# Performance work log

Measured on AMD Instinct MI355X. Metric: run time of the kernel, lower is better.

The kernel has to match this reference:

```python
import jax, jax.numpy as jnp
import numpy as np

EPS = 1e-5
K = 9  # 3x3 kernel taps


def _deform_conv_bn_relu(x, w_off, b_off, w, gamma, beta):
    B, C, H, W = x.shape
    dt = x.dtype
    # offset-predicting conv: [B, 2*K, H, W], channel layout (y,x) pairs per tap (mmcv v1)
    offset = jax.lax.conv_general_dilated(
        x, w_off, window_strides=(1, 1), padding=((1, 1), (1, 1)),
        dimension_numbers=('NCHW', 'OIHW', 'NCHW')) + b_off[None, :, None, None]
    off = offset.reshape(B, K, 2, H, W)
    # kernel tap displacements relative to output pixel (padding=1 -> centered 3x3)
    dy = (jnp.arange(K) // 3 - 1).astype(dt)
    dx = (jnp.arange(K) % 3 - 1).astype(dt)
    ii = jnp.arange(H, dtype=dt)[:, None]
    jj = jnp.arange(W, dtype=dt)[None, :]
    py = ii[None, None] + dy[None, :, None, None] + off[:, :, 0]  # [B,K,H,W]
    px = jj[None, None] + dx[None, :, None, None] + off[:, :, 1]
    y0 = jnp.floor(py)
    x0 = jnp.floor(px)
    ly = py - y0
    lx = px - x0

    xf = x.reshape(B, C, H * W)

    def gather(yc, xc, wt):
        # bilinear corner gather with zero padding outside the image
        valid = (yc >= 0) & (yc < H) & (xc >= 0) & (xc < W)
        yi = jnp.clip(yc, 0, H - 1).astype(jnp.int32)
        xi = jnp.clip(xc, 0, W - 1).astype(jnp.int32)
        idx = (yi * W + xi).reshape(B, -1)              # [B, K*H*W]
        g = jax.vmap(lambda xb, ib: xb[:, ib])(xf, idx)  # [B, C, K*H*W]
        wm = (wt * valid.astype(dt)).reshape(B, 1, -1)
        return g * wm

    val = (gather(y0, x0, (1 - ly) * (1 - lx))
           + gather(y0, x0 + 1, (1 - ly) * lx)
           + gather(y0 + 1, x0, ly * (1 - lx))
           + gather(y0 + 1, x0 + 1, ly * lx))
    val = val.reshape(B, C, K, H, W)

    # deformable conv accumulation (no bias in mmcv DeformConv2d v1)
    O = w.shape[0]
    out = jnp.einsum('ock,bckhw->bohw', w.reshape(O, C, K), val)

    # BatchNorm (training-mode batch stats) + ReLU
    mean = out.mean(axis=(0, 2, 3))
    var = out.var(axis=(0, 2, 3))
    out = (out - mean[None, :, None, None]) * jax.lax.rsqrt(var + EPS)[None, :, None, None]
    out = out * gamma[None, :, None, None] + beta[None, :, None, None]
    return jax.nn.relu(out)


def setup_inputs() -> dict:
    key = jax.random.key(0)
    k1, k2, k3 = jax.random.split(key, 3)
    B, C, O, H, W = 2, 256, 256, 128, 128
    x = jax.random.normal(k1, (B, C, H, W), dtype=jnp.float32)
    # offset branch: small init so predicted offsets stay in a realistic range
    w_off = jax.random.normal(k2, (2 * K, C, 3, 3), dtype=jnp.float32) * 0.01
    b_off = jnp.zeros((2 * K,), dtype=jnp.float32)
    w = jax.random.normal(k3, (O, C, 3, 3), dtype=jnp.float32) * 0.05
    gamma = jnp.ones((O,), dtype=jnp.float32)
    beta = jnp.zeros((O,), dtype=jnp.float32)
    return {"x": x, "w_off": w_off, "b_off": b_off, "w": w, "gamma": gamma, "beta": beta}


def reference(x, w_off, b_off, w, gamma, beta):
    return _deform_conv_bn_relu(x, w_off, b_off, w, gamma, beta)
```

## Files before the change

kernel.cpp:

```cpp
#include <hip/hip_runtime.h>
#include <hip/hip_bf16.h>

#define HWs   16384
#define Wimg  128
#define Himg  128
#define PW    130
#define PHW   16900
#define Cin   256
#define Oout  256
#define CKd   2304
#define Bb    2

typedef short   bf16x8 __attribute__((ext_vector_type(8)));
typedef float   f32x4  __attribute__((ext_vector_type(4)));

__device__ __forceinline__ float bf2f(ushort u){
  union { unsigned int i; float f; } v; v.i = ((unsigned int)u) << 16; return v.f;
}
__device__ __forceinline__ ushort f2bf(float f){
  union { float f; unsigned int i; } v; v.f = f;
  return (ushort)((v.i + 0x8000u) >> 16);
}
__device__ __forceinline__ unsigned cvt_pk_bf16(float lo, float hi){
  unsigned r;
  asm("v_cvt_pk_bf16_f32 %0, %1, %2" : "=v"(r) : "v"(lo), "v"(hi));
  return r;
}
__device__ __forceinline__ void gload_lds16(const ushort* g, void* l){
  __builtin_amdgcn_global_load_lds(
      (const __attribute__((address_space(1))) unsigned int*)g,
      (__attribute__((address_space(3))) unsigned int*)l, 16, 0, 0);
}

__global__ __launch_bounds__(256) void k_transpose(const float* __restrict__ x,
                                                   ushort* __restrict__ xtp){
  int bx = blockIdx.x;
  int b  = bx >> 10;
  int r  = bx & 1023;
  int ct = r >> 8;
  int pt = r & 255;
  int c0 = ct * 64, p0 = pt * 64;
  __shared__ float tile[64][65];
  const float* xb = x + (size_t)b * Cin * HWs;
  #pragma unroll
  for (int pass = 0; pass < 16; ++pass){
    int idx = pass * 256 + threadIdx.x;
    int cl = idx >> 6, pl = idx & 63;
    tile[cl][pl] = xb[(size_t)(c0 + cl) * HWs + p0 + pl];
  }
  __syncthreads();
  ushort* xo = xtp + (size_t)b * PHW * Cin;
  #pragma unroll
  for (int pass = 0; pass < 16; ++pass){
    int idx = pass * 256 + threadIdx.x;
    int pl = idx >> 6, cl = idx & 63;
    int hw = p0 + pl; int y = hw >> 7, xc = hw & 127;
    xo[(size_t)((y + 1) * PW + xc + 1) * Cin + c0 + cl] = f2bf(tile[cl][pl]);
  }
}

__global__ __launch_bounds__(64) void k_border(ushort* __restrict__ xtp){
  int e = blockIdx.x;
  int b = e / 516, p = e % 516;
  int y, xc;
  if (p < 130)      { y = 0;       xc = p; }
  else if (p < 260) { y = 129;     xc = p - 130; }
  else if (p < 388) { y = p - 259; xc = 0; }
  else              { y = p - 387; xc = 129; }
  uint2* dst = (uint2*)(xtp + ((size_t)b * PHW + y * PW + xc) * Cin) + threadIdx.x;
  *dst = make_uint2(0u, 0u);
}

__global__ __launch_bounds__(256) void k_wprep(const float* __restrict__ w,
                                               const float* __restrict__ wof,
                                               ushort* __restrict__ w2,
                                               ushort* __restrict__ w2of){
  int idx = blockIdx.x * 256 + threadIdx.x;
  if (idx < Oout * CKd){
    int o = idx / CKd, r = idx % CKd;
    int k = r >> 8, c = r & 255;
    w2[idx] = f2bf(w[(size_t)(o * Cin + c) * 9 + k]);
  } else {
    int j = idx - Oout * CKd;
    int o = j / CKd, r = j % CKd;
    int k = r >> 8, c = r & 255;
    float v = (o < 18) ? wof[(size_t)(o * Cin + c) * 9 + k] : 0.f;
    w2of[j] = f2bf(v);
  }
}

__global__ __launch_bounds__(512, 4) void k_offconv(const ushort* __restrict__ xtp,
                                                    const ushort* __restrict__ w2of,
                                                    const float* __restrict__ b_off,
                                                    int4* __restrict__ pidx,
                                                    float4* __restrict__ pw){
  int bx = blockIdx.x;
  int blkm = ((bx & 7) << 6) | (bx >> 3);
  int b = blkm >> 8, tile = blkm & 255;
  int hw0 = tile * 64;
  int iy = tile >> 1, jx0 = (tile & 1) * 64;
  __shared__ __align__(16) ushort aw[2][2048];
  __shared__ __align__(16) ushort bv_s[2][4096];
  __shared__ float offs_lds[18][64];
  int t = threadIdx.x, lane = t & 63, wid = t >> 6;
  int mi = wid >> 2, ni = wid & 3;
  f32x4 acc = (f32x4){0,0,0,0};
  const ushort* xb = xtp + (size_t)b * PHW * Cin;

#define OSTAGE(S, P) \
  if ((S) < 36){ int kks = (S) * 64, kt = (S) >> 2, c0s = ((S) * 64) & 255; \
    int dy = kt / 3 - 1, dxx = kt % 3 - 1; \
    if (wid < 4){ int L = t * 16; int oo = L >> 7; int inb = (L & 127) ^ ((oo & 7) << 4); \
      gload_lds16(w2of + (size_t)oo * CKd + kks + (inb >> 1), (char*)aw[P] + L); } \
    { int L = t * 16; int hw_l = L >> 7; int inb = (L & 127) ^ ((hw_l & 7) << 4); \
      int row = (iy + dy + 1) * PW + (jx0 + hw_l + dxx + 1); \
      gload_lds16(xb + (size_t)row * Cin + c0s + (inb >> 1), (char*)bv_s[P] + L); } }

  OSTAGE(0, 0);
  __syncthreads();
  #pragma unroll 1
  for (int step = 0; step < 36; ++step){
    int P = step & 1;
    OSTAGE(step + 1, P ^ 1);
    #pragma unroll
    for (int kk2 = 0; kk2 < 2; ++kk2){
      int coff = kk2 * 64 + ((lane >> 4) << 4);
      bf16x8 a0, bb;
      { int r = mi * 16 + (lane & 15); int byte = r * 128 + coff; byte ^= ((r & 7) << 4); a0 = *(const bf16x8*)((char*)aw[P] + byte); }
      { int r = ni * 16 + (lane & 15); int byte = r * 128 + coff; byte ^= ((r & 7) << 4); bb = *(const bf16x8*)((char*)bv_s[P] + byte); }
      acc = __builtin_amdgcn_mfma_f32_16x16x32_bf16(a0, bb, acc, 0, 0, 0);
    }
    __syncthreads();
  }
#undef OSTAGE
  {
    int hw_l = ni * 16 + (lane & 15);
    #pragma unroll
    for (int r = 0; r < 4; ++r){
      int o = mi * 16 + ((lane >> 4) << 2) + r;
      if (o < 18) offs_lds[o][hw_l] = acc[r] + b_off[o];
    }
  }
  __syncthreads();
  for (int idx = t; idx < 9 * 64; idx += 512){
    int k = idx >> 6, jl = idx & 63;
    int hw = hw0 + jl;
    int i = hw >> 7, jcol = hw & 127;
    float offy = offs_lds[2 * k][jl];
    float offx = offs_lds[2 * k + 1][jl];
    float py = (float)i    + (float)(k / 3 - 1) + offy;
    float px = (float)jcol + (float)(k % 3 - 1) + offx;
    float y0f = floorf(py), x0f = floorf(px);
    float ly = py - y0f, lx = px - x0f;
    int y0 = (int)y0f, x0 = (int)x0f;
    int y1 = y0 + 1, x1 = x0 + 1;
    float w00 = (1.f - ly) * (1.f - lx), w01 = (1.f - ly) * lx;
    float w10 = ly * (1.f - lx),         w11 = ly * lx;
    bool vy0 = (y0 >= 0 && y0 < 128), vy1 = (y1 >= 0 && y1 < 128);
    bool vx0 = (x0 >= 0 && x0 < 128), vx1 = (x1 >= 0 && x1 < 128);
    int iy0 = min(max(y0, 0), 127), iy1 = min(max(y1, 0), 127);
    int ix0 = min(max(x0, 0), 127), ix1 = min(max(x1, 0), 127);
    size_t e = ((size_t)b * 9 + k) * HWs + hw;
    pidx[e] = make_int4(((iy0 + 1) * PW + ix0 + 1) * Cin, ((iy0 + 1) * PW + ix1 + 1) * Cin,
                        ((iy1 + 1) * PW + ix0 + 1) * Cin, ((iy1 + 1) * PW + ix1 + 1) * Cin);
    pw[e]   = make_float4(vy0 && vx0 ? w00 : 0.f, vy0 && vx1 ? w01 : 0.f,
                          vy1 && vx0 ? w10 : 0.f, vy1 && vx1 ? w11 : 0.f);
  }
}

__device__ __forceinline__ unsigned combine_pair(unsigned d0, unsigned d1, unsigned d2, unsigned d3,
                                                 float4 wt){
  float e0 = wt.x * __uint_as_float(d0 << 16)
           + wt.y * __uint_as_float(d1 << 16)
           + wt.z * __uint_as_float(d2 << 16)
           + wt.w * __uint_as_float(d3 << 16);
  float e1 = wt.x * __uint_as_float(d0 & 0xFFFF0000u)
           + wt.y * __uint_as_float(d1 & 0xFFFF0000u)
           + wt.z * __uint_as_float(d2 & 0xFFFF0000u)
           + wt.w * __uint_as_float(d3 & 0xFFFF0000u);
  return cvt_pk_bf16(e0, e1);
}

__global__ __launch_bounds__(512, 2) void k_main(const ushort* __restrict__ xtp,
                                                 const ushort* __restrict__ w2,
                                                 const int4* __restrict__ pidx,
                                                 const float4* __restrict__ pw,
                                                 float* __restrict__ out,
                                                 float* __restrict__ partials){
  int bx = blockIdx.x;
  int blkm = ((bx & 7) << 5) | (bx >> 3);
  int b = blkm >> 7, tile = blkm & 127;
  int hw0 = tile * 128;
  __shared__ __align__(16) ushort smem[49152];
  ushort* Ab0 = smem;
  ushort* Ab1 = smem + 16384;
  ushort* Bb0 = smem + 32768;
  ushort* Bb1 = smem + 40960;
  int t = threadIdx.x, lane = t & 63, wid = t >> 6;
  int wm = wid >> 1, wn = wid & 1;
  int cg = t & 7, hl = t >> 3;
  f32x4 acc[4][4];
  #pragma unroll
  for (int mi = 0; mi < 4; ++mi)
    #pragma unroll
    for (int ni = 0; ni < 4; ++ni) acc[mi][ni] = (f32x4){0,0,0,0};
  const ushort* xb  = xtp  + (size_t)b * PHW * Cin;
  const int4*   pib = pidx + (size_t)b * 9 * HWs + hw0;
  const float4* pwb = pw   + (size_t)b * 9 * HWs + hw0;

  int4   ids[2][2];
  float4 wts[2][2];
  uint4  g[2][2][4];

#define IDSLOAD(P, S) \
  if ((S) < 36){ int kq = (S) >> 2; \
    ids[P][0] = pib[(size_t)kq * HWs + hl]; \
    ids[P][1] = pib[(size_t)kq * HWs + hl + 64]; }

#define CORNERS(P, S) \
  if ((S) < 36){ int cb = (((S) * 64) & 255) + cg * 8; int kq = (S) >> 2; \
    wts[P][0] = pwb[(size_t)kq * HWs + hl]; \
    wts[P][1] = pwb[(size_t)kq * HWs + hl + 64]; \
    _Pragma("unroll") for (int hh = 0; hh < 2; ++hh){ \
      g[P][hh][0] = *(const uint4*)(xb + ids[P][hh].x + cb); \
      g[P][hh][1] = *(const uint4*)(xb + ids[P][hh].y + cb); \
      g[P][hh][2] = *(const uint4*)(xb + ids[P][hh].z + cb); \
      g[P][hh][3] = *(const uint4*)(xb + ids[P][hh].w + cb); } }

#define STAGEA(S, ABP) \
  if ((S) < 36){ int kks = (S) * 64; \
    _Pragma("unroll") for (int h2 = 0; h2 < 4; ++h2){ \
      int L = (wid * 4 + h2) * 1024 + lane * 16; \
      int oo = L >> 7; int inb = (L & 127) ^ ((oo & 7) << 4); \
      gload_lds16(w2 + (size_t)oo * CKd + kks + (inb >> 1), (char*)(ABP) + L); } }

#define COMBINE(P, S, BBP) \
  if ((S) < 36){ \
    _Pragma("unroll") for (int hh = 0; hh < 2; ++hh){ \
      int hw_l = hl + hh * 64; \
      float4 wtv = wts[P][hh]; \
      uint4 ov; \
      ov.x = combine_pair(g[P][hh][0].x, g[P][hh][1].x, g[P][hh][2].x, g[P][hh][3].x, wtv); \
      ov.y = combine_pair(g[P][hh][0].y, g[P][hh][1].y, g[P][hh][2].y, g[P][hh][3].y, wtv); \
      ov.z = combine_pair(g[P][hh][0].z, g[P][hh][1].z, g[P][hh][2].z, g[P][hh][3].z, wtv); \
      ov.w = combine_pair(g[P][hh][0].w, g[P][hh][1].w, g[P][hh][2].w, g[P][hh][3].w, wtv); \
      int byte = hw_l * 128 + cg * 16; byte ^= ((hw_l & 7) << 4); \
      *(uint4*)((char*)(BBP) + byte) = ov; } }

#define MFMA_PHASE(ABP, BBP) \
  { __builtin_amdgcn_s_setprio(1); \
    _Pragma("unroll") for (int kk2 = 0; kk2 < 2; ++kk2){ \
      int coff = kk2 * 64 + ((lane >> 4) << 4); \
      bf16x8 a[4], bv[4]; \
      _Pragma("unroll") for (int mi = 0; mi < 4; ++mi){ \
        int r = wm * 64 + mi * 16 + (lane & 15); \
        int byte = r * 128 + coff; byte ^= ((r & 7) << 4); \
        a[mi] = *(const bf16x8*)((const char*)(ABP) + byte); } \
      _Pragma("unroll") for (int ni = 0; ni < 4; ++ni){ \
        int r = wn * 64 + ni * 16 + (lane & 15); \
        int byte = r * 128 + coff; byte ^= ((r & 7) << 4); \
        bv[ni] = *(const bf16x8*)((const char*)(BBP) + byte); } \
      _Pragma("unroll") for (int mi = 0; mi < 4; ++mi) \
        _Pragma("unroll") for (int ni = 0; ni < 4; ++ni) \
          acc[mi][ni] = __builtin_amdgcn_mfma_f32_16x16x32_bf16(a[mi], bv[ni], acc[mi][ni], 0, 0, 0); } \
    __builtin_amdgcn_s_setprio(0); }

  IDSLOAD(0, 0);
  IDSLOAD(1, 1);
  CORNERS(0, 0);
  IDSLOAD(0, 2);
  CORNERS(1, 1);
  IDSLOAD(1, 3);
  STAGEA(0, Ab0);
  COMBINE(0, 0, Bb0);
  __syncthreads();

  #pragma unroll 1
  for (int tt = 0; tt < 36; tt += 2){
    CORNERS(0, tt + 2);
    STAGEA(tt + 1, Ab1);
    IDSLOAD(0, tt + 4);
    MFMA_PHASE(Ab0, Bb0);
    COMBINE(1, tt + 1, Bb1);
    __syncthreads();
    CORNERS(1, tt + 3);
    STAGEA(tt + 2, Ab0);
    IDSLOAD(1, tt + 5);
    MFMA_PHASE(Ab1, Bb1);
    COMBINE(0, tt + 2, Bb0);
    __syncthreads();
  }
#undef IDSLOAD
#undef CORNERS
#undef STAGEA
#undef COMBINE
#undef MFMA_PHASE

  #pragma unroll
  for (int mi = 0; mi < 4; ++mi){
    int obase = wm * 64 + mi * 16 + ((lane >> 4) << 2);
    #pragma unroll
    for (int ni = 0; ni < 4; ++ni){
      int hw = hw0 + wn * 64 + ni * 16 + (lane & 15);
      float* op = out + ((size_t)b * Oout + obase) * HWs + hw;
      #pragma unroll
      for (int r = 0; r < 4; ++r) op[(size_t)r * HWs] = acc[mi][ni][r];
    }
  }
  #pragma unroll
  for (int mi = 0; mi < 4; ++mi){
    #pragma unroll
    for (int r = 0; r < 4; ++r){
      float s = 0.f, s2 = 0.f;
      #pragma unroll
      for (int ni = 0; ni < 4; ++ni){ float v = acc[mi][ni][r]; s += v; s2 += v * v; }
      #pragma unroll
      for (int off2 = 1; off2 < 16; off2 <<= 1){
        s  += __shfl_xor(s, off2);
        s2 += __shfl_xor(s2, off2);
      }
      if ((lane & 15) == 0){
        int o = wm * 64 + mi * 16 + ((lane >> 4) << 2) + r;
        int row = blkm * 2 + wn;
        partials[(size_t)row * 256 + o] = s;
        partials[(size_t)512 * 256 + (size_t)row * 256 + o] = s2;
      }
    }
  }
}

__global__ __launch_bounds__(256) void k_bnstats(const float* __restrict__ partials,
                                                 float* __restrict__ stats){
  int o = blockIdx.x, t = threadIdx.x;
  float s = 0.f, s2 = 0.f;
  for (int i = t; i < 512; i += 256){
    s  += partials[(size_t)i * 256 + o];
    s2 += partials[(size_t)512 * 256 + (size_t)i * 256 + o];
  }
  #pragma unroll
  for (int off = 32; off > 0; off >>= 1){
    s  += __shfl_down(s, off);
    s2 += __shfl_down(s2, off);
  }
  __shared__ float rs[4], rs2[4];
  int lane = t & 63, w = t >> 6;
  if (lane == 0){ rs[w] = s; rs2[w] = s2; }
  __syncthreads();
  if (t == 0){
    float S = 0.f, S2 = 0.f;
    for (int i = 0; i < 4; ++i){ S += rs[i]; S2 += rs2[i]; }
    float mean = S / 32768.f;
    float var  = S2 / 32768.f - mean * mean;
    stats[o] = mean;
    stats[256 + o] = rsqrtf(var + 1e-5f);
  }
}

__global__ __launch_bounds__(256) void k_bnapply(float* __restrict__ out,
                                                 const float* __restrict__ stats,
                                                 const float* __restrict__ gamma,
                                                 const float* __restrict__ beta){
  size_t e = ((size_t)blockIdx.x * 256 + threadIdx.x) * 4;
  int o = (int)((e >> 14) & 255);
  float mean = stats[o], rstd = stats[256 + o];
  float sc = rstd * gamma[o];
  float sh = beta[o] - mean * sc;
  float4 v = *(float4*)(out + e);
  v.x = fmaxf(v.x * sc + sh, 0.f);
  v.y = fmaxf(v.y * sc + sh, 0.f);
  v.z = fmaxf(v.z * sc + sh, 0.f);
  v.w = fmaxf(v.w * sc + sh, 0.f);
  *(float4*)(out + e) = v;
}

extern "C" void kernel_launch(void* const* d_in, const int* in_sizes, int n_in,
                              void* d_out, int out_size, void* d_ws, size_t ws_size,
                              hipStream_t stream){
  const float* x     = (const float*)d_in[0];
  const float* w_off = (const float*)d_in[1];
  const float* b_off = (const float*)d_in[2];
  const float* w     = (const float*)d_in[3];
  const float* gamma = (const float*)d_in[4];
  const float* beta  = (const float*)d_in[5];
  float* out = (float*)d_out;

  char* p = (char*)d_ws;
  ushort* xtp  = (ushort*)p; p += (size_t)Bb * PHW * Cin * 2;
  ushort* w2   = (ushort*)p; p += (size_t)Oout * CKd * 2;
  ushort* w2of = (ushort*)p; p += (size_t)32 * CKd * 2;
  int4*   pidx = (int4*)p;   p += (size_t)Bb * 9 * HWs * 16;
  float4* pwt  = (float4*)p; p += (size_t)Bb * 9 * HWs * 16;
  float*  parts= (float*)p;  p += (size_t)2 * 512 * 256 * 4;
  float*  stats= (float*)p;

  k_transpose<<<dim3(2048), dim3(256), 0, stream>>>(x, xtp);
  k_border   <<<dim3(1032), dim3(64),  0, stream>>>(xtp);
  k_wprep    <<<dim3(2592), dim3(256), 0, stream>>>(w, w_off, w2, w2of);
  k_offconv  <<<dim3(512),  dim3(512), 0, stream>>>(xtp, w2of, b_off, pidx, pwt);
  k_main     <<<dim3(256),  dim3(512), 0, stream>>>(xtp, w2, pidx, pwt, out, parts);
  k_bnstats  <<<dim3(256),  dim3(256), 0, stream>>>(parts, stats);
  k_bnapply  <<<dim3(8192), dim3(256), 0, stream>>>(out, stats, gamma, beta);
}
```

Before: 126.0 us.

## Double k_main block to 1024 threads, halving per-thread gather and MFMA work

The main deformable-conv GEMM kernel now launches 1024 threads (16 waves in a 4x4 wave grid) instead of 512. Each thread gathers one pixel instead of two and holds a 4x2 accumulator tile instead of 4x4. The BN partials buffer and the stats reduction grow to 1024 rows to match. The aim is more waves in flight to hide gather latency and lower register pressure, at the cost of less B-fragment reuse per wave and more LDS reads per MFMA.

```diff
diff --git a/kernel.cpp b/kernel.cpp
--- a/kernel.cpp
+++ b/kernel.cpp
@@ -181,12 +181,12 @@
   return cvt_pk_bf16(e0, e1);
 }
 
-__global__ __launch_bounds__(512, 2) void k_main(const ushort* __restrict__ xtp,
-                                                 const ushort* __restrict__ w2,
-                                                 const int4* __restrict__ pidx,
-                                                 const float4* __restrict__ pw,
-                                                 float* __restrict__ out,
-                                                 float* __restrict__ partials){
+__global__ __launch_bounds__(1024, 4) void k_main(const ushort* __restrict__ xtp,
+                                                  const ushort* __restrict__ w2,
+                                                  const int4* __restrict__ pidx,
+                                                  const float4* __restrict__ pw,
+                                                  float* __restrict__ out,
+                                                  float* __restrict__ partials){
   int bx = blockIdx.x;
   int blkm = ((bx & 7) << 5) | (bx >> 3);
   int b = blkm >> 7, tile = blkm & 127;
@@ -197,71 +197,66 @@
   ushort* Bb0 = smem + 32768;
   ushort* Bb1 = smem + 40960;
   int t = threadIdx.x, lane = t & 63, wid = t >> 6;
-  int wm = wid >> 1, wn = wid & 1;
+  int wm = wid >> 2, wn = wid & 3;
   int cg = t & 7, hl = t >> 3;
-  f32x4 acc[4][4];
+  f32x4 acc[4][2];
   #pragma unroll
   for (int mi = 0; mi < 4; ++mi)
     #pragma unroll
-    for (int ni = 0; ni < 4; ++ni) acc[mi][ni] = (f32x4){0,0,0,0};
+    for (int ni = 0; ni < 2; ++ni) acc[mi][ni] = (f32x4){0,0,0,0};
   const ushort* xb  = xtp  + (size_t)b * PHW * Cin;
   const int4*   pib = pidx + (size_t)b * 9 * HWs + hw0;
   const float4* pwb = pw   + (size_t)b * 9 * HWs + hw0;
 
-  int4   ids[2][2];
-  float4 wts[2][2];
-  uint4  g[2][2][4];
+  int4   ids[2];
+  float4 wts[2];
+  uint4  g[2][4];
 
 #define IDSLOAD(P, S) \
   if ((S) < 36){ int kq = (S) >> 2; \
-    ids[P][0] = pib[(size_t)kq * HWs + hl]; \
-    ids[P][1] = pib[(size_t)kq * HWs + hl + 64]; }
+    ids[P] = pib[(size_t)kq * HWs + hl]; }
 
 #define CORNERS(P, S) \
   if ((S) < 36){ int cb = (((S) * 64) & 255) + cg * 8; int kq = (S) >> 2; \
-    wts[P][0] = pwb[(size_t)kq * HWs + hl]; \
-    wts[P][1] = pwb[(size_t)kq * HWs + hl + 64]; \
-    _Pragma("unroll") for (int hh = 0; hh < 2; ++hh){ \
-      g[P][hh][0] = *(const uint4*)(xb + ids[P][hh].x + cb); \
-      g[P][hh][1] = *(const uint4*)(xb + ids[P][hh].y + cb); \
-      g[P][hh][2] = *(const uint4*)(xb + ids[P][hh].z + cb); \
-      g[P][hh][3] = *(const uint4*)(xb + ids[P][hh].w + cb); } }
+    wts[P] = pwb[(size_t)kq * HWs + hl]; \
+    g[P][0] = *(const uint4*)(xb + ids[P].x + cb); \
+    g[P][1] = *(const uint4*)(xb + ids[P].y + cb); \
+    g[P][2] = *(const uint4*)(xb + ids[P].z + cb); \
+    g[P][3] = *(const uint4*)(xb + ids[P].w + cb); }
 
 #define STAGEA(S, ABP) \
   if ((S) < 36){ int kks = (S) * 64; \
-    _Pragma("unroll") for (int h2 = 0; h2 < 4; ++h2){ \
-      int L = (wid * 4 + h2) * 1024 + lane * 16; \
+    _Pragma("unroll") for (int h2 = 0; h2 < 2; ++h2){ \
+      int L = (wid * 2 + h2) * 1024 + lane * 16; \
       int oo = L >> 7; int inb = (L & 127) ^ ((oo & 7) << 4); \
       gload_lds16(w2 + (size_t)oo * CKd + kks + (inb >> 1), (char*)(ABP) + L); } }
 
 #define COMBINE(P, S, BBP) \
   if ((S) < 36){ \
-    _Pragma("unroll") for (int hh = 0; hh < 2; ++hh){ \
-      int hw_l = hl + hh * 64; \
-      float4 wtv = wts[P][hh]; \
-      uint4 ov; \
-      ov.x = combine_pair(g[P][hh][0].x, g[P][hh][1].x, g[P][hh][2].x, g[P][hh][3].x, wtv); \
-      ov.y = combine_pair(g[P][hh][0].y, g[P][hh][1].y, g[P][hh][2].y, g[P][hh][3].y, wtv); \
-      ov.z = combine_pair(g[P][hh][0].z, g[P][hh][1].z, g[P][hh][2].z, g[P][hh][3].z, wtv); \
-      ov.w = combine_pair(g[P][hh][0].w, g[P][hh][1].w, g[P][hh][2].w, g[P][hh][3].w, wtv); \
-      int byte = hw_l * 128 + cg * 16; byte ^= ((hw_l & 7) << 4); \
-      *(uint4*)((char*)(BBP) + byte) = ov; } }
+    float4 wtv = wts[P]; \
+    uint4 ov; \
+    ov.x = combine_pair(g[P][0].x, g[P][1].x, g[P][2].x, g[P][3].x, wtv); \
+    ov.y = combine_pair(g[P][0].y, g[P][1].y, g[P][2].y, g[P][3].y, wtv); \
+    ov.z = combine_pair(g[P][0].z, g[P][1].z, g[P][2].z, g[P][3].z, wtv); \
+    ov.w = combine_pair(g[P][0].w, g[P][1].w, g[P][2].w, g[P][3].w, wtv); \
+    int byte = hl * 128 + cg * 16; byte ^= ((hl & 7) << 4); \
+    *(uint4*)((char*)(BBP) + byte) = ov; }
 
 #define MFMA_PHASE(ABP, BBP) \
   { __builtin_amdgcn_s_setprio(1); \
     _Pragma("unroll") for (int kk2 = 0; kk2 < 2; ++kk2){ \
       int coff = kk2 * 64 + ((lane >> 4) << 4); \
-      bf16x8 a[4], bv[4]; \
+      bf16x8 a[4], bv[2]; \
       _Pragma("unroll") for (int mi = 0; mi < 4; ++mi){ \
         int r = wm * 64 + mi * 16 + (lane & 15); \
         int byte = r * 128 + coff; byte ^= ((r & 7) << 4); \
         a[mi] = *(const bf16x8*)((const char*)(ABP) + byte); } \
-      _Pragma("unroll") for (int ni = 0; ni < 4; ++ni){ \
-        int r = wn * 64 + ni * 16 + (lane & 15); \
+      _Pragma("unroll") for (int ni = 0; ni < 2; ++ni){ \
+        int r = wn * 32 + ni * 16 + (lane & 15); \
         int byte = r * 128 + coff; byte ^= ((r & 7) << 4); \
         bv[ni] = *(const bf16x8*)((const char*)(BBP) + byte); } \
       _Pragma("unroll") for (int mi = 0; mi < 4; ++mi) \
-        _Pragma("unroll") for (int ni = 0; ni < 4; ++ni) \
+        _Pragma("unroll") for (int ni = 0; ni < 2; ++ni) \
           acc[mi][ni] = __builtin_amdgcn_mfma_f32_16x16x32_bf16(a[mi], bv[ni], acc[mi][ni], 0, 0, 0); } \
     __builtin_amdgcn_s_setprio(0); }
 
@@ -300,8 +295,8 @@
   for (int mi = 0; mi < 4; ++mi){
     int obase = wm * 64 + mi * 16 + ((lane >> 4) << 2);
     #pragma unroll
-    for (int ni = 0; ni < 4; ++ni){
-      int hw = hw0 + wn * 64 + ni * 16 + (lane & 15);
+    for (int ni = 0; ni < 2; ++ni){
+      int hw = hw0 + wn * 32 + ni * 16 + (lane & 15);
       float* op = out + ((size_t)b * Oout + obase) * HWs + hw;
       #pragma unroll
       for (int r = 0; r < 4; ++r) op[(size_t)r * HWs] = acc[mi][ni][r];
@@ -313,7 +308,7 @@
     for (int r = 0; r < 4; ++r){
       float s = 0.f, s2 = 0.f;
       #pragma unroll
-      for (int ni = 0; ni < 4; ++ni){ float v = acc[mi][ni][r]; s += v; s2 += v * v; }
+      for (int ni = 0; ni < 2; ++ni){ float v = acc[mi][ni][r]; s += v; s2 += v * v; }
       #pragma unroll
       for (int off2 = 1; off2 < 16; off2 <<= 1){
         s  += __shfl_xor(s, off2);
@@ -321,9 +316,9 @@
       }
       if ((lane & 15) == 0){
         int o = wm * 64 + mi * 16 + ((lane >> 4) << 2) + r;
-        int row = blkm * 2 + wn;
+        int row = blkm * 4 + wn;
         partials[(size_t)row * 256 + o] = s;
-        partials[(size_t)512 * 256 + (size_t)row * 256 + o] = s2;
+        partials[(size_t)1024 * 256 + (size_t)row * 256 + o] = s2;
       }
     }
   }
@@ -333,9 +328,9 @@
                                                  float* __restrict__ stats){
   int o = blockIdx.x, t = threadIdx.x;
   float s = 0.f, s2 = 0.f;
-  for (int i = t; i < 512; i += 256){
+  for (int i = t; i < 1024; i += 256){
     s  += partials[(size_t)i * 256 + o];
-    s2 += partials[(size_t)512 * 256 + (size_t)i * 256 + o];
+    s2 += partials[(size_t)1024 * 256 + (size_t)i * 256 + o];
   }
   #pragma unroll
   for (int off = 32; off > 0; off >>= 1){
@@ -390,14 +385,14 @@
   ushort* w2of = (ushort*)p; p += (size_t)32 * CKd * 2;
   int4*   pidx = (int4*)p;   p += (size_t)Bb * 9 * HWs * 16;
   float4* pwt  = (float4*)p; p += (size_t)Bb * 9 * HWs * 16;
-  float*  parts= (float*)p;  p += (size_t)2 * 512 * 256 * 4;
+  float*  parts= (float*)p;  p += (size_t)2 * 1024 * 256 * 4;
   float*  stats= (float*)p;
 
   k_transpose<<<dim3(2048), dim3(256), 0, stream>>>(x, xtp);
   k_border   <<<dim3(1032), dim3(64),  0, stream>>>(xtp);
   k_wprep    <<<dim3(2592), dim3(256), 0, stream>>>(w, w_off, w2, w2of);
   k_offconv  <<<dim3(512),  dim3(512), 0, stream>>>(xtp, w2of, b_off, pidx, pwt);
-  k_main     <<<dim3(256),  dim3(512), 0, stream>>>(xtp, w2, pidx, pwt, out, parts);
+  k_main     <<<dim3(256),  dim3(1024), 0, stream>>>(xtp, w2, pidx, pwt, out, parts);
   k_bnstats  <<<dim3(256),  dim3(256), 0, stream>>>(parts, stats);
   k_bnapply  <<<dim3(8192), dim3(256), 0, stream>>>(out, stats, gamma, beta);
 }
```

Result: no change. 125.4 us (-0.4%).
